# Kernel optimization log

Hardware: AMD Instinct MI355X
Metric: run time of the kernel (lower is better)

The kernel has to match this reference:

```python
import jax, jax.numpy as jnp
import numpy as np

COMMITMENT_COST = 0.25


def setup_inputs() -> dict:
    key = jax.random.key(0)
    k1, k2 = jax.random.split(key)
    x = jax.random.normal(k1, (32, 256, 32, 32), dtype=jnp.float32)
    codebook = jax.random.normal(k2, (1024, 256), dtype=jnp.float32) * 0.02
    return {"x": x, "codebook": codebook}


def reference(x, codebook):
    # x: [B, C, H, W] -> z: [B, H, W, C] (NHWC), C = embedding_dim
    B, C, H, W = x.shape
    z = jnp.transpose(x, (0, 2, 3, 1))
    zf = z.reshape(-1, C)  # [N, C], N = B*H*W
    # squared euclidean distance: ||z||^2 - 2 z.e + ||e||^2  -> [N, K]
    d = (
        jnp.sum(zf * zf, axis=-1, keepdims=True)
        - 2.0 * (zf @ codebook.T)
        + jnp.sum(codebook * codebook, axis=-1)
    )
    encoding_indices = jnp.argmin(d, axis=1)  # [N]
    quantized = codebook[encoding_indices].reshape(z.shape)  # [B, H, W, C]

    # training losses (entropy_loss_ratio == 0 -> entropy branch skipped)
    sg = jax.lax.stop_gradient
    e_latent_loss = jnp.mean((sg(quantized) - z) ** 2) * COMMITMENT_COST
    q_latent_loss = jnp.mean((quantized - sg(z)) ** 2)
    quantizer_loss = e_latent_loss + q_latent_loss

    # straight-through estimator
    quantized_st = z + sg(quantized - z)
    out = jnp.transpose(quantized_st, (0, 3, 1, 2))  # back to NCHW
    return out, quantizer_loss, e_latent_loss, q_latent_loss, encoding_indices
```

## Files before the change

kernel.cpp:

```cpp
#include <hip/hip_runtime.h>
#include <cfloat>

#define C_DIM   256
#define HW      1024
#define N_ROWS  32768
#define K_CODES 1024
#define ROWS    64
#define NSUPER  16
#define SUPER_BYTES 32768
#define LISTCAP 128
#define DELTA   0.008f
#define CMASK   0xFFFFFFF0u
#define ZSTRIDE 260

#define OUT_ELEMS 8388608
#define LOSS_OFF  8388608
#define IDX_OFF   8388611

typedef _Float16 half8 __attribute__((ext_vector_type(8)));
typedef _Float16 f16x4 __attribute__((ext_vector_type(4)));
typedef float    f32x4 __attribute__((ext_vector_type(4)));

#define AS1 __attribute__((address_space(1)))
#define AS3 __attribute__((address_space(3)))

#define OFF_EBUF  0
#define OFF_EN    66560
#define OFF_S32   70656
#define OFF_M1W   70912
#define OFF_THR   71936
#define OFF_RES   72192
#define OFF_FIDX  72704
#define OFF_LCNT  72960
#define OFF_LMETA 73216
#define SMEM_BYTES 77312

#define QT_STRIDE 258

#define DPP_MIN(x, ctrl) fminf((x), __int_as_float(__builtin_amdgcn_update_dpp(0, __float_as_int(x), (ctrl), 0xf, 0xf, true)))

__global__ void prep_kernel(const float* __restrict__ cb, float* __restrict__ enorm,
                            char* __restrict__ cb16) {
    int k = blockIdx.x * 4 + (threadIdx.x >> 6);
    int lane = threadIdx.x & 63;
    int c0 = lane * 4;
    float4 v = *(const float4*)(cb + k * C_DIM + c0);
    double s = (double)v.x * v.x + (double)v.y * v.y + (double)v.z * v.z + (double)v.w * v.w;
    #pragma unroll
    for (int m = 1; m < 64; m <<= 1) s += __shfl_xor(s, m, 64);
    if (lane == 0) enorm[k] = (float)s;
    f16x4 h;
    h[0] = (_Float16)v.x; h[1] = (_Float16)v.y; h[2] = (_Float16)v.z; h[3] = (_Float16)v.w;
    int dst = ((k >> 4) << 13) + ((c0 >> 5) << 10) + (((c0 >> 3) & 3) << 8)
            + ((k & 15) << 4) + ((c0 & 7) << 1);
    *(f16x4*)(cb16 + dst) = h;
}

__global__ __launch_bounds__(512, 4) void vq_main(
    const float* __restrict__ x, const float* __restrict__ cb,
    const float* __restrict__ enorm_g, const char* __restrict__ cb16,
    float* __restrict__ out, float* __restrict__ idx_out, float* __restrict__ t2_out)
{
    extern __shared__ char smem[];
    float* zt      = (float*)(smem + OFF_EBUF);
    float* qt      = (float*)(smem + OFF_EBUF);
    char*  ebuf    = smem + OFF_EBUF;
    float* en_lds  = (float*)(smem + OFF_EN);
    float* S32     = (float*)(smem + OFF_S32);
    float* m1w     = (float*)(smem + OFF_M1W);
    float* thr     = (float*)(smem + OFF_THR);
    unsigned long long* res = (unsigned long long*)(smem + OFF_RES);
    int*   fidx    = (int*)(smem + OFF_FIDX);
    int*   lcnt    = (int*)(smem + OFF_LCNT);
    unsigned int* lmeta = (unsigned int*)(smem + OFF_LMETA);

    const int t    = threadIdx.x;
    const int lane = t & 63;
    const int wv   = t >> 6;
    const int wr   = wv >> 2;
    const int wq   = wv & 3;
    const int l15  = lane & 15;
    const int l4   = lane >> 4;
    const int row0 = blockIdx.x * ROWS;
    const int b    = row0 >> 10;
    const int hw0  = row0 & 1023;
    const float* xb = x + b * (C_DIM * HW) + hw0;

    const int qofs = wv * 4096;

    {
        int g   = t & 15;
        int cb4 = t >> 4;
        for (int cc = cb4 * 4; cc < C_DIM; cc += 128) {
            float4 v0 = *(const float4*)(xb + (cc + 0) * HW + g * 4);
            float4 v1 = *(const float4*)(xb + (cc + 1) * HW + g * 4);
            float4 v2 = *(const float4*)(xb + (cc + 2) * HW + g * 4);
            float4 v3 = *(const float4*)(xb + (cc + 3) * HW + g * 4);
            *(float4*)&zt[(g * 4 + 0) * ZSTRIDE + cc] = make_float4(v0.x, v1.x, v2.x, v3.x);
            *(float4*)&zt[(g * 4 + 1) * ZSTRIDE + cc] = make_float4(v0.y, v1.y, v2.y, v3.y);
            *(float4*)&zt[(g * 4 + 2) * ZSTRIDE + cc] = make_float4(v0.z, v1.z, v2.z, v3.z);
            *(float4*)&zt[(g * 4 + 3) * ZSTRIDE + cc] = make_float4(v0.w, v1.w, v2.w, v3.w);
        }
        if (t < 256) *(float4*)&en_lds[t * 4] = *(const float4*)(enorm_g + t * 4);
        if (t < 8) lcnt[t] = 0;
    }
    __syncthreads();

    if (t < 256) {
        int r = t >> 2, seg = t & 3;
        const float* zr = &zt[r * ZSTRIDE + seg * 64];
        double s = 0.0;
        for (int c = 0; c < 64; c += 4) {
            float4 v = *(const float4*)(zr + c);
            s = fma((double)v.x, (double)v.x, s);
            s = fma((double)v.y, (double)v.y, s);
            s = fma((double)v.z, (double)v.z, s);
            s = fma((double)v.w, (double)v.w, s);
        }
        s += __shfl_xor(s, 1, 64);
        s += __shfl_xor(s, 2, 64);
        if (seg == 0) S32[r] = (float)s;
    }

    half8 af[2][8];
    #pragma unroll
    for (int rt = 0; rt < 2; rt++) {
        int row = wr * 32 + rt * 16 + l15;
        #pragma unroll
        for (int kk = 0; kk < 8; kk++) {
            int c0 = kk * 32 + l4 * 8;
            float4 a  = *(const float4*)&zt[row * ZSTRIDE + c0];
            float4 a2 = *(const float4*)&zt[row * ZSTRIDE + c0 + 4];
            half8 h;
            h[0] = (_Float16)(-2.0f * a.x);  h[1] = (_Float16)(-2.0f * a.y);
            h[2] = (_Float16)(-2.0f * a.z);  h[3] = (_Float16)(-2.0f * a.w);
            h[4] = (_Float16)(-2.0f * a2.x); h[5] = (_Float16)(-2.0f * a2.y);
            h[6] = (_Float16)(-2.0f * a2.z); h[7] = (_Float16)(-2.0f * a2.w);
            af[rt][kk] = h;
        }
    }
    __syncthreads();

    #pragma unroll
    for (int i = 0; i < 4; i++) {
        __builtin_amdgcn_global_load_lds((const AS1 unsigned int*)(cb16 + qofs + i * 1024 + lane * 16),
                                         (AS3 unsigned int*)(ebuf + qofs + i * 1024), 16, 0, 0);
    }

    const int bbase  = (wq << 13) + (l4 << 8) + (l15 << 4);
    const int enbase = wq * 16 + l15;

    float u1[2][4], u2[2][4];
    #pragma unroll
    for (int rt = 0; rt < 2; rt++)
        #pragma unroll
        for (int r2 = 0; r2 < 4; r2++) { u1[rt][r2] = FLT_MAX; u2[rt][r2] = FLT_MAX; }

    for (int sc = 0; sc < NSUPER; sc++) {
        asm volatile("s_waitcnt vmcnt(0)" ::: "memory");
        __builtin_amdgcn_sched_barrier(0);
        __builtin_amdgcn_s_barrier();
        __builtin_amdgcn_sched_barrier(0);

        const char* ebc = ebuf + (sc & 1) * SUPER_BYTES;

        if (sc + 1 < NSUPER) {
            const char* src = cb16 + (sc + 1) * SUPER_BYTES + qofs;
            char* dst = ebuf + ((sc + 1) & 1) * SUPER_BYTES + qofs;
            #pragma unroll
            for (int i = 0; i < 4; i++) {
                __builtin_amdgcn_global_load_lds((const AS1 unsigned int*)(src + i * 1024 + lane * 16),
                                                 (AS3 unsigned int*)(dst + i * 1024), 16, 0, 0);
            }
        }

        const float en = en_lds[enbase + sc * 64];
        f32x4 acc0 = {en, en, en, en};
        f32x4 acc1 = {en, en, en, en};
        {
            half8 bf[4];
            #pragma unroll
            for (int kk = 0; kk < 4; kk++)
                bf[kk] = *(const half8*)(ebc + bbase + (kk << 10));
            #pragma unroll
            for (int kk = 0; kk < 4; kk++) {
                acc0 = __builtin_amdgcn_mfma_f32_16x16x32_f16(af[0][kk], bf[kk], acc0, 0, 0, 0);
                acc1 = __builtin_amdgcn_mfma_f32_16x16x32_f16(af[1][kk], bf[kk], acc1, 0, 0, 0);
            }
        }
        {
            half8 bf[4];
            #pragma unroll
            for (int kk = 0; kk < 4; kk++)
                bf[kk] = *(const half8*)(ebc + bbase + ((kk + 4) << 10));
            #pragma unroll
            for (int kk = 0; kk < 4; kk++) {
                acc0 = __builtin_amdgcn_mfma_f32_16x16x32_f16(af[0][kk + 4], bf[kk], acc0, 0, 0, 0);
                acc1 = __builtin_amdgcn_mfma_f32_16x16x32_f16(af[1][kk + 4], bf[kk], acc1, 0, 0, 0);
            }
        }

        #pragma unroll
        for (int r2 = 0; r2 < 4; r2++) {
            float a0 = __uint_as_float((__float_as_uint(acc0[r2]) & CMASK) | (unsigned)sc);
            u2[0][r2] = __builtin_amdgcn_fmed3f(a0, u1[0][r2], u2[0][r2]);
            u1[0][r2] = fminf(u1[0][r2], a0);
            float a1 = __uint_as_float((__float_as_uint(acc1[r2]) & CMASK) | (unsigned)sc);
            u2[1][r2] = __builtin_amdgcn_fmed3f(a1, u1[1][r2], u2[1][r2]);
            u1[1][r2] = fminf(u1[1][r2], a1);
        }
    }

    #pragma unroll
    for (int rt = 0; rt < 2; rt++) {
        #pragma unroll
        for (int r2 = 0; r2 < 4; r2++) {
            float m = u1[rt][r2];
            m = DPP_MIN(m, 0xB1);
            m = DPP_MIN(m, 0x4E);
            m = DPP_MIN(m, 0x141);
            m = DPP_MIN(m, 0x140);
            if (l15 == 0) m1w[wq * 64 + wr * 32 + rt * 16 + l4 * 4 + r2] = m;
        }
    }
    __syncthreads();
    if (t < 64) {
        thr[t] = fminf(fminf(m1w[t], m1w[64 + t]), fminf(m1w[128 + t], m1w[192 + t])) + DELTA;
        res[t] = ~0ull;
    }
    __syncthreads();

    #pragma unroll
    for (int rt = 0; rt < 2; rt++) {
        #pragma unroll
        for (int r2 = 0; r2 < 4; r2++) {
            int row_l = wr * 32 + rt * 16 + l4 * 4 + r2;
            float tr = thr[row_l];
            if (u1[rt][r2] < tr) {
                int sc1 = (int)(__float_as_uint(u1[rt][r2]) & 15u);
                int code = sc1 * 64 + wq * 16 + l15;
                int slot = atomicAdd(&lcnt[wv], 1);
                if (slot < LISTCAP)
                    lmeta[wv * LISTCAP + slot] = ((unsigned)row_l << 16) | (unsigned)code;
            }
            if (u2[rt][r2] < tr) {
                int sc2 = (int)(__float_as_uint(u2[rt][r2]) & 15u);
                int code = sc2 * 64 + wq * 16 + l15;
                int slot = atomicAdd(&lcnt[wv], 1);
                if (slot < LISTCAP)
                    lmeta[wv * LISTCAP + slot] = ((unsigned)row_l << 16) | (unsigned)code;
            }
        }
    }
    __syncthreads();

    {
        int n = lcnt[wv]; if (n > LISTCAP) n = LISTCAP;
        for (int base = 0; base < n; base += 4) {
            int it = base + l4;
            if (it < n) {
                unsigned meta = lmeta[wv * LISTCAP + it];
                int row  = (int)(meta >> 16);
                int code = (int)(meta & 1023u);
                const float* xr = xb + row;
                const float* er = cb + code * C_DIM;
                double acc = 0.0;
                #pragma unroll
                for (int s2 = 0; s2 < 16; s2++) {
                    int c = l15 + 16 * s2;
                    acc = fma((double)xr[(size_t)c * HW], (double)er[c], acc);
                }
                acc += __shfl_xor(acc, 1, 64);
                acc += __shfl_xor(acc, 2, 64);
                acc += __shfl_xor(acc, 4, 64);
                acc += __shfl_xor(acc, 8, 64);
                if (l15 == 0) {
                    float Mf = (float)acc;
                    float t2 = __fadd_rn(__fsub_rn(S32[row], __fmul_rn(2.0f, Mf)), en_lds[code]);
                    unsigned long long pk =
                        ((unsigned long long)__float_as_uint(t2) << 32) | (unsigned long long)(unsigned)code;
                    atomicMin(&res[row], pk);
                }
            }
        }
    }
    __syncthreads();

    if (t < 64) {
        unsigned long long v = res[t];
        int code = (int)(v & 1023u);
        fidx[t] = code;
        idx_out[row0 + t] = (float)code;
        t2_out[row0 + t] = __uint_as_float((unsigned)(v >> 32));
    }

    float* ob = out + b * (C_DIM * HW) + hw0;
    #pragma unroll
    for (int half = 0; half < 2; half++) {
        __syncthreads();
        for (int idx = t; idx < 32 * 64; idx += 512) {
            int r  = idx >> 6;
            int c4 = idx & 63;
            const float* er = cb + fidx[half * 32 + r] * C_DIM;
            *(float4*)&qt[r * QT_STRIDE + c4 * 4] = *(const float4*)(er + c4 * 4);
        }
        __syncthreads();
        int rr = t & 31;
        int cg = t >> 5;
        for (int cc = cg; cc < C_DIM; cc += 16) {
            ob[cc * HW + half * 32 + rr] = qt[rr * QT_STRIDE + cc];
        }
    }
}

__global__ void loss_kernel(const float* __restrict__ t2min, float* __restrict__ losses) {
    __shared__ double sh[256];
    int t = threadIdx.x;
    double a = 0.0;
    const int per = N_ROWS / 256;
    for (int i = t * per; i < t * per + per; i++) a += (double)t2min[i];
    sh[t] = a;
    __syncthreads();
    for (int s = 128; s > 0; s >>= 1) {
        if (t < s) sh[t] += sh[t + s];
        __syncthreads();
    }
    if (t == 0) {
        double M = sh[0] / (double)OUT_ELEMS;
        losses[0] = (float)(1.25 * M);
        losses[1] = (float)(0.25 * M);
        losses[2] = (float)(M);
    }
}

extern "C" void kernel_launch(void* const* d_in, const int* in_sizes, int n_in,
                              void* d_out, int out_size, void* d_ws, size_t ws_size,
                              hipStream_t stream) {
    const float* x  = (const float*)d_in[0];
    const float* cb = (const float*)d_in[1];
    float* out     = (float*)d_out;
    float* losses  = out + LOSS_OFF;
    float* idx_out = out + IDX_OFF;

    char*  cb16     = (char*)d_ws;
    float* t2ws     = (float*)((char*)d_ws + 524288);
    float* enorm_ws = (float*)((char*)d_ws + 524288 + 131072);

    hipFuncSetAttribute(reinterpret_cast<const void*>(vq_main),
                        hipFuncAttributeMaxDynamicSharedMemorySize, SMEM_BYTES);

    prep_kernel<<<K_CODES / 4, 256, 0, stream>>>(cb, enorm_ws, cb16);
    vq_main<<<N_ROWS / ROWS, 512, SMEM_BYTES, stream>>>(x, cb, enorm_ws, cb16, out, idx_out, t2ws);
    loss_kernel<<<1, 256, 0, stream>>>(t2ws, losses);
}
```

Before: 65.66 us.

## Split VQ kernel into sweep and finish kernels via workspace candidate lists

```diff
diff --git a/kernel.cpp b/kernel.cpp
--- a/kernel.cpp
+++ b/kernel.cpp
@@ -29,13 +29,17 @@
 #define OFF_S32   70656
 #define OFF_M1W   70912
 #define OFF_THR   71936
-#define OFF_RES   72192
-#define OFF_FIDX  72704
-#define OFF_LCNT  72960
-#define OFF_LMETA 73216
-#define SMEM_BYTES 77312
+#define OFF_LCNT  72192
+#define SMEM_A    72448
 
 #define QT_STRIDE 258
+
+#define WS_CB16   0
+#define WS_T2     524288
+#define WS_EN     655360
+#define WS_S32    659456
+#define WS_LCNT   790528
+#define WS_LMETA  806912
 
 #define DPP_MIN(x, ctrl) fminf((x), __int_as_float(__builtin_amdgcn_update_dpp(0, __float_as_int(x), (ctrl), 0xf, 0xf, true)))
 
@@ -56,23 +60,19 @@
     *(f16x4*)(cb16 + dst) = h;
 }
 
-__global__ __launch_bounds__(512, 4) void vq_main(
-    const float* __restrict__ x, const float* __restrict__ cb,
-    const float* __restrict__ enorm_g, const char* __restrict__ cb16,
-    float* __restrict__ out, float* __restrict__ idx_out, float* __restrict__ t2_out)
+__global__ __launch_bounds__(512, 4) void vq_sweep(
+    const float* __restrict__ x, const float* __restrict__ enorm_g,
+    const char* __restrict__ cb16, float* __restrict__ S32_g,
+    int* __restrict__ lcnt_g, unsigned int* __restrict__ lmeta_g)
 {
     extern __shared__ char smem[];
     float* zt      = (float*)(smem + OFF_EBUF);
-    float* qt      = (float*)(smem + OFF_EBUF);
     char*  ebuf    = smem + OFF_EBUF;
     float* en_lds  = (float*)(smem + OFF_EN);
     float* S32     = (float*)(smem + OFF_S32);
     float* m1w     = (float*)(smem + OFF_M1W);
     float* thr     = (float*)(smem + OFF_THR);
-    unsigned long long* res = (unsigned long long*)(smem + OFF_RES);
-    int*   fidx    = (int*)(smem + OFF_FIDX);
     int*   lcnt    = (int*)(smem + OFF_LCNT);
-    unsigned int* lmeta = (unsigned int*)(smem + OFF_LMETA);
 
     const int t    = threadIdx.x;
     const int lane = t & 63;
@@ -81,7 +81,8 @@
     const int wq   = wv & 3;
     const int l15  = lane & 15;
     const int l4   = lane >> 4;
-    const int row0 = blockIdx.x * ROWS;
+    const int blk  = blockIdx.x;
+    const int row0 = blk * ROWS;
     const int b    = row0 >> 10;
     const int hw0  = row0 & 1023;
     const float* xb = x + b * (C_DIM * HW) + hw0;
@@ -119,7 +120,7 @@
         }
         s += __shfl_xor(s, 1, 64);
         s += __shfl_xor(s, 2, 64);
-        if (seg == 0) S32[r] = (float)s;
+        if (seg == 0) { S32[r] = (float)s; S32_g[blk * 64 + r] = (float)s; }
     }
 
     half8 af[2][8];
@@ -224,12 +225,11 @@
         }
     }
     __syncthreads();
-    if (t < 64) {
+    if (t < 64)
         thr[t] = fminf(fminf(m1w[t], m1w[64 + t]), fminf(m1w[128 + t], m1w[192 + t])) + DELTA;
-        res[t] = ~0ull;
-    }
-    __syncthreads();
-
+    __syncthreads();
+
+    unsigned int* lmb = lmeta_g + blk * (8 * LISTCAP) + wv * LISTCAP;
     #pragma unroll
     for (int rt = 0; rt < 2; rt++) {
         #pragma unroll
@@ -240,26 +240,53 @@
                 int sc1 = (int)(__float_as_uint(u1[rt][r2]) & 15u);
                 int code = sc1 * 64 + wq * 16 + l15;
                 int slot = atomicAdd(&lcnt[wv], 1);
-                if (slot < LISTCAP)
-                    lmeta[wv * LISTCAP + slot] = ((unsigned)row_l << 16) | (unsigned)code;
+                if (slot < LISTCAP) lmb[slot] = ((unsigned)row_l << 16) | (unsigned)code;
             }
             if (u2[rt][r2] < tr) {
                 int sc2 = (int)(__float_as_uint(u2[rt][r2]) & 15u);
                 int code = sc2 * 64 + wq * 16 + l15;
                 int slot = atomicAdd(&lcnt[wv], 1);
-                if (slot < LISTCAP)
-                    lmeta[wv * LISTCAP + slot] = ((unsigned)row_l << 16) | (unsigned)code;
-            }
-        }
-    }
-    __syncthreads();
-
-    {
-        int n = lcnt[wv]; if (n > LISTCAP) n = LISTCAP;
-        for (int base = 0; base < n; base += 4) {
-            int it = base + l4;
+                if (slot < LISTCAP) lmb[slot] = ((unsigned)row_l << 16) | (unsigned)code;
+            }
+        }
+    }
+    __syncthreads();
+    if (t < 8) {
+        int n = lcnt[t]; if (n > LISTCAP) n = LISTCAP;
+        lcnt_g[blk * 8 + t] = n;
+    }
+}
+
+__global__ __launch_bounds__(256) void vq_finish(
+    const float* __restrict__ x, const float* __restrict__ cb,
+    const float* __restrict__ enorm_g, const float* __restrict__ S32_g,
+    const int* __restrict__ lcnt_g, const unsigned int* __restrict__ lmeta_g,
+    float* __restrict__ out, float* __restrict__ idx_out, float* __restrict__ t2_out)
+{
+    __shared__ __align__(16) float qt[32 * QT_STRIDE];
+    __shared__ float S32l[64];
+    __shared__ unsigned long long res[64];
+    __shared__ int fidx[64];
+
+    const int t    = threadIdx.x;
+    const int grp  = t >> 4;
+    const int l15  = t & 15;
+    const int blk  = blockIdx.x;
+    const int row0 = blk * ROWS;
+    const int b    = row0 >> 10;
+    const int hw0  = row0 & 1023;
+    const float* xb = x + b * (C_DIM * HW) + hw0;
+
+    if (t < 64) { S32l[t] = S32_g[blk * 64 + t]; res[t] = ~0ull; }
+    __syncthreads();
+
+    const unsigned int* lmb = lmeta_g + blk * (8 * LISTCAP);
+    for (int wseg = 0; wseg < 8; wseg++) {
+        int n = lcnt_g[blk * 8 + wseg];
+        for (int base = 0; base < n; base += 16) {
+            int it = base + grp;
             if (it < n) {
-                unsigned meta = lmeta[wv * LISTCAP + it];
+                unsigned meta = lmb[wseg * LISTCAP + it];
                 int row  = (int)(meta >> 16);
                 int code = (int)(meta & 1023u);
                 const float* xr = xb + row;
@@ -276,7 +303,7 @@
                 acc += __shfl_xor(acc, 8, 64);
                 if (l15 == 0) {
                     float Mf = (float)acc;
-                    float t2 = __fadd_rn(__fsub_rn(S32[row], __fmul_rn(2.0f, Mf)), en_lds[code]);
+                    float t2 = __fadd_rn(__fsub_rn(S32l[row], __fmul_rn(2.0f, Mf)), enorm_g[code]);
                     unsigned long long pk =
                         ((unsigned long long)__float_as_uint(t2) << 32) | (unsigned long long)(unsigned)code;
                     atomicMin(&res[row], pk);
@@ -298,7 +325,7 @@
     #pragma unroll
     for (int half = 0; half < 2; half++) {
         __syncthreads();
-        for (int idx = t; idx < 32 * 64; idx += 512) {
+        for (int idx = t; idx < 32 * 64; idx += 256) {
             int r  = idx >> 6;
             int c4 = idx & 63;
             const float* er = cb + fidx[half * 32 + r] * C_DIM;
@@ -307,7 +334,7 @@
         __syncthreads();
         int rr = t & 31;
         int cg = t >> 5;
-        for (int cc = cg; cc < C_DIM; cc += 16) {
+        for (int cc = cg; cc < C_DIM; cc += 8) {
             ob[cc * HW + half * 32 + rr] = qt[rr * QT_STRIDE + cc];
         }
     }
@@ -342,14 +369,20 @@
     float* losses  = out + LOSS_OFF;
     float* idx_out = out + IDX_OFF;
 
-    char*  cb16     = (char*)d_ws;
-    float* t2ws     = (float*)((char*)d_ws + 524288);
-    float* enorm_ws = (float*)((char*)d_ws + 524288 + 131072);
-
-    hipFuncSetAttribute(reinterpret_cast<const void*>(vq_main),
-                        hipFuncAttributeMaxDynamicSharedMemorySize, SMEM_BYTES);
+    char* ws = (char*)d_ws;
+    char*  cb16     = ws + WS_CB16;
+    float* t2ws     = (float*)(ws + WS_T2);
+    float* enorm_ws = (float*)(ws + WS_EN);
+    float* S32_g    = (float*)(ws + WS_S32);
+    int*   lcnt_g   = (int*)(ws + WS_LCNT);
+    unsigned int* lmeta_g = (unsigned int*)(ws + WS_LMETA);
+
+    hipFuncSetAttribute(reinterpret_cast<const void*>(vq_sweep),
+                        hipFuncAttributeMaxDynamicSharedMemorySize, SMEM_A);
 
     prep_kernel<<<K_CODES / 4, 256, 0, stream>>>(cb, enorm_ws, cb16);
-    vq_main<<<N_ROWS / ROWS, 512, SMEM_BYTES, stream>>>(x, cb, enorm_ws, cb16, out, idx_out, t2ws);
+    vq_sweep<<<N_ROWS / ROWS, 512, SMEM_A, stream>>>(x, enorm_ws, cb16, S32_g, lcnt_g, lmeta_g);
+    vq_finish<<<N_ROWS / ROWS, 256, 0, stream>>>(x, cb, enorm_ws, S32_g, lcnt_g, lmeta_g,
+                                                 out, idx_out, t2ws);
     loss_kernel<<<1, 256, 0, stream>>>(t2ws, losses);
 }
```

Result: slower. 75.28 us (+14.7%).
